# Optimization experiments

Measured on AMD Instinct MI355X. Metric: run time of the kernel, lower is better.

## Reference

```python
import jax, jax.numpy as jnp
import numpy as np

IMAGE_SIZE = 224
IN_CH = 3
A = -0.5
GLIMPSE_SIZES = [12, 23, 68, 135]  # ceil(224 * s) for s in [0.05, 0.1, 0.3, 0.6]
PAD = (GLIMPSE_SIZES[-1] - 1) // 2  # 67
G0 = GLIMPSE_SIZES[0]  # 12 -> all glimpses resized to 12x12
KSIZES = [sz - G0 + 1 for sz in GLIMPSE_SIZES]  # [1, 12, 57, 124]
BATCH = 256


def _bicubic_kernel(sz, a=A, in_ch=IN_CH, out_ch=1):
    # faithful to GlimpseSensor.init (learn_kernels=False)
    x = np.arange(-sz / 2.0 + 0.5, sz / 2.0 + 0.5)[:, None] * 2.0 / sz * (2.0 if sz > 2.0 else 1.0)
    x = np.abs(x)
    w = np.where(
        x > 2.0,
        0.0,
        np.where(
            x > 1.0,
            a * x**3 - 5.0 * a * x**2 + 8.0 * a * x - 4.0 * a,
            (a + 2.0) * x**3 - (a + 3.0) * x**2 + 1.0,
        ),
    )
    k = w @ w.T  # (sz, sz)
    k = k * out_ch / (in_ch * k.sum())
    return np.broadcast_to(k, (out_ch, in_ch, sz, sz)).astype(np.float32)


def setup_inputs() -> dict:
    key = jax.random.key(0)
    ki, kl = jax.random.split(key)
    imgs = jax.random.normal(ki, (BATCH, IN_CH, IMAGE_SIZE, IMAGE_SIZE), dtype=jnp.float32)
    locs = jax.random.randint(kl, (BATCH, 2), 0, IMAGE_SIZE)
    d = {"imgs": imgs, "locs": locs}
    for i, sz in enumerate(KSIZES):
        d[f"k{i}"] = jnp.asarray(_bicubic_kernel(sz))
    return d


def _crop(padded_img, loc, g):
    # padded_img: (C, H+2p, W+2p); loc = (x, y); crop rows [p+x-g//2, p+x+(g+1)//2)
    start = (0, PAD + loc[0] - g // 2, PAD + loc[1] - g // 2)
    return jax.lax.dynamic_slice(padded_img, start, (padded_img.shape[0], g, g))


def reference(imgs, locs, k0, k1, k2, k3):
    p = PAD
    padded = jnp.pad(imgs, ((0, 0), (0, 0), (p, p), (p, p)))  # zero padding, as in forward
    kernels = [k0, k1, k2, k3]
    outs = []
    for g, k in zip(GLIMPSE_SIZES, kernels):
        crops = jax.vmap(lambda img, loc: _crop(img, loc, g))(padded, locs)  # (B, C, g, g)
        out = jax.lax.conv_general_dilated(
            crops, k, window_strides=(1, 1), padding='VALID',
            dimension_numbers=('NCHW', 'OIHW', 'NCHW'),
        )  # (B, 1, 12, 12)
        outs.append(out)
    return jnp.concatenate(outs, axis=1)  # (B, num_glimpses, 12, 12)
```

## Files before the change

### kernel.cpp

```cpp
#include <hip/hip_runtime.h>

namespace {

constexpr int IMGSZ = 224;
constexpr int IMG2  = IMGSZ * IMGSZ;

template <int G>
__device__ void chunk_glimpse(
    int b, int gi, int ch,
    const float* __restrict__ img, const int* __restrict__ locs,
    const float* __restrict__ kptr, float* __restrict__ out,
    float (*s_lds)[136], float* vpad, float* upad,
    float (*part2)[16][13], float (*h_lds)[12]) {
  constexpr int KSZ = G - 11;
  constexpr int C0  = KSZ / 2;
  constexpr int G4  = (G + 3) & ~3;
  constexpr int NCB = G4 / 4;
  const int tid = threadIdx.x;
  const int r0 = ch * 16;

  {
    const float rpiv = 1.0f / kptr[C0 * KSZ + C0];
    for (int i = tid; i < 160; i += 128) {
      float v = 0.f;
      const int k = i - 11;
      if (k >= 0 && k < KSZ) v = kptr[C0 * KSZ + k] * rpiv;
      vpad[i] = v;
    }
  }
  for (int i = tid; i < 160; i += 128) {
    float u = 0.f;
    const int j = i - 16;
    if (j >= 0 && j < KSZ) u = kptr[j * KSZ + C0];
    upad[i] = u;
  }

  const int x = locs[2 * b];
  const int y = locs[2 * b + 1];
  const int row0 = x - G / 2 + r0;
  const int col0 = y - G / 2;
  const int R = (G - r0) < 16 ? (G - r0) : 16;
  const float* imgb = img + (size_t)b * (3 * IMG2);

  for (int idx = tid; idx < 16 * G4; idx += 128) {
    const int r = idx / G4;
    const int c = idx - r * G4;
    float s = 0.f;
    if (r < R && c < G) {
      const int row = row0 + r;
      const int col = col0 + c;
      if ((unsigned)row < (unsigned)IMGSZ && (unsigned)col < (unsigned)IMGSZ) {
        const float* p = imgb + row * IMGSZ + col;
        s = p[0] + p[IMG2] + p[2 * IMG2];
      }
    }
    s_lds[r][c] = s;
  }
  __syncthreads();

  const int row = tid & 15;
  const int seg = tid >> 4;
  float acc[12];
  #pragma unroll
  for (int i = 0; i < 12; ++i) acc[i] = 0.f;

  for (int cb = seg; cb < NCB; cb += 8) {
    const int c = cb * 4;
    const float4 s4 = *reinterpret_cast<const float4*>(&s_lds[row][c]);
    float vv[16];
    #pragma unroll
    for (int q = 0; q < 4; ++q) {
      const float4 v4 = *reinterpret_cast<const float4*>(&vpad[c + q * 4]);
      vv[q * 4 + 0] = v4.x; vv[q * 4 + 1] = v4.y; vv[q * 4 + 2] = v4.z; vv[q * 4 + 3] = v4.w;
    }
    const float sj[4] = {s4.x, s4.y, s4.z, s4.w};
    #pragma unroll
    for (int j = 0; j < 4; ++j) {
      #pragma unroll
      for (int ox = 0; ox < 12; ++ox) {
        acc[ox] += sj[j] * vv[11 + j - ox];
      }
    }
  }

  #pragma unroll
  for (int ox = 0; ox < 12; ++ox) {
    acc[ox] += __shfl_down(acc[ox], 32, 64);
    acc[ox] += __shfl_down(acc[ox], 16, 64);
  }
  const int lane = tid & 63;
  const int wv = tid >> 6;
  if (lane < 16) {
    #pragma unroll
    for (int ox = 0; ox < 12; ++ox) part2[wv][lane][ox] = acc[ox];
  }
  __syncthreads();
  for (int e = tid; e < 192; e += 128) {
    const int r = e / 12;
    const int ox = e - r * 12;
    h_lds[r][ox] = (r < R) ? (part2[0][r][ox] + part2[1][r][ox]) : 0.f;
  }
  __syncthreads();

  float* outp = out + ((size_t)b * 4 + gi) * 144;
  #pragma unroll
  for (int pass = 0; pass < 2; ++pass) {
    const int e = tid + pass * 128;
    if (e < 144) {
      const int oy = e / 12;
      const int ox = e - oy * 12;
      float s = 0.f;
      #pragma unroll
      for (int r = 0; r < 16; ++r) {
        s += upad[16 + r0 + r - oy] * h_lds[r][ox];
      }
      atomicAdd(&outp[e], s);
    }
  }
}

__global__ __launch_bounds__(128) void glimpse_kernel(
    const float* __restrict__ img, const int* __restrict__ locs,
    const float* __restrict__ k0, const float* __restrict__ k1,
    const float* __restrict__ k2, const float* __restrict__ k3,
    float* __restrict__ out) {
  __shared__ __align__(16) float s_lds[16][136];
  __shared__ __align__(16) float vpad[160];
  __shared__ __align__(16) float upad[160];
  __shared__ float part2[2][16][13];
  __shared__ float h_lds[16][12];
  const int bid = blockIdx.x;
  const int b = bid & 255;
  const int t = bid >> 8;
  if (t == 0) {
    chunk_glimpse<12 >(b, 0, 0,     img, locs, k0, out, s_lds, vpad, upad, part2, h_lds);
  } else if (t < 3) {
    chunk_glimpse<23 >(b, 1, t - 1, img, locs, k1, out, s_lds, vpad, upad, part2, h_lds);
  } else if (t < 8) {
    chunk_glimpse<68 >(b, 2, t - 3, img, locs, k2, out, s_lds, vpad, upad, part2, h_lds);
  } else {
    chunk_glimpse<135>(b, 3, t - 8, img, locs, k3, out, s_lds, vpad, upad, part2, h_lds);
  }
}

}

extern "C" void kernel_launch(void* const* d_in, const int* in_sizes, int n_in,
                              void* d_out, int out_size, void* d_ws, size_t ws_size,
                              hipStream_t stream) {
  const float* img  = (const float*)d_in[0];
  const int*   locs = (const int*)d_in[1];
  const float* k0   = (const float*)d_in[2];
  const float* k1   = (const float*)d_in[3];
  const float* k2   = (const float*)d_in[4];
  const float* k3   = (const float*)d_in[5];
  float* out = (float*)d_out;

  hipMemsetAsync(out, 0, (size_t)out_size * sizeof(float), stream);
  glimpse_kernel<<<256 * 17, 128, 0, stream>>>(img, locs, k0, k1, k2, k3, out);
}
```

Before: 28.05 us.

## Load image rows directly from global with aligned float4 and make waves independent

The block-wide LDS staging of the channel-summed crop is replaced by per-thread aligned float4 loads straight from global memory. The horizontal kernel vector is pre-shifted by the column misalignment so the loads can be 16-byte aligned, with a scalar path at image edges. Each wave now keeps its own copies of the kernel vectors and the row buffer and issues its own atomicAdds, which removes every __syncthreads in exchange for twice as many atomics per output. A minimum-occupancy hint is also added to the launch bounds.

```diff
diff --git a/kernel.cpp b/kernel.cpp
--- a/kernel.cpp
+++ b/kernel.cpp
@@ -10,75 +10,80 @@
     int b, int gi, int ch,
     const float* __restrict__ img, const int* __restrict__ locs,
     const float* __restrict__ kptr, float* __restrict__ out,
-    float (*s_lds)[136], float* vpad, float* upad,
-    float (*part2)[16][13], float (*h_lds)[12]) {
-  constexpr int KSZ = G - 11;
-  constexpr int C0  = KSZ / 2;
-  constexpr int G4  = (G + 3) & ~3;
-  constexpr int NCB = G4 / 4;
-  const int tid = threadIdx.x;
+    float* __restrict__ vpad2, float* __restrict__ upad,
+    float (*__restrict__ h_lds)[12]) {
+  constexpr int KSZ  = G - 11;
+  constexpr int C0   = KSZ / 2;
+  constexpr int NCB2 = (G + 2) / 4 + 1;
+  const int lane = threadIdx.x & 63;
   const int r0 = ch * 16;
-
-  {
-    const float rpiv = 1.0f / kptr[C0 * KSZ + C0];
-    for (int i = tid; i < 160; i += 128) {
-      float v = 0.f;
-      const int k = i - 11;
-      if (k >= 0 && k < KSZ) v = kptr[C0 * KSZ + k] * rpiv;
-      vpad[i] = v;
-    }
-  }
-  for (int i = tid; i < 160; i += 128) {
-    float u = 0.f;
-    const int j = i - 16;
-    if (j >= 0 && j < KSZ) u = kptr[j * KSZ + C0];
-    upad[i] = u;
-  }
 
   const int x = locs[2 * b];
   const int y = locs[2 * b + 1];
   const int row0 = x - G / 2 + r0;
   const int col0 = y - G / 2;
+  const int sh = col0 & 3;
+  const int col_a0 = col0 - sh;
   const int R = (G - r0) < 16 ? (G - r0) : 16;
   const float* imgb = img + (size_t)b * (3 * IMG2);
 
-  for (int idx = tid; idx < 16 * G4; idx += 128) {
-    const int r = idx / G4;
-    const int c = idx - r * G4;
-    float s = 0.f;
-    if (r < R && c < G) {
-      const int row = row0 + r;
-      const int col = col0 + c;
-      if ((unsigned)row < (unsigned)IMGSZ && (unsigned)col < (unsigned)IMGSZ) {
-        const float* p = imgb + row * IMGSZ + col;
-        s = p[0] + p[IMG2] + p[2 * IMG2];
-      }
+  {
+    const float rpiv = 1.0f / kptr[C0 * KSZ + C0];
+    for (int i = lane; i < 176; i += 64) {
+      const int k = i - 11 - sh;
+      vpad2[i] = (k >= 0 && k < KSZ) ? kptr[C0 * KSZ + k] * rpiv : 0.f;
     }
-    s_lds[r][c] = s;
   }
-  __syncthreads();
+  for (int i = lane; i < 160; i += 64) {
+    const int j = i - 16;
+    upad[i] = (j >= 0 && j < KSZ) ? kptr[j * KSZ + C0] : 0.f;
+  }
 
-  const int row = tid & 15;
-  const int seg = tid >> 4;
+  const int row = lane & 15;
+  const int seg = (threadIdx.x >> 6) * 4 + (lane >> 4);
+
   float acc[12];
   #pragma unroll
   for (int i = 0; i < 12; ++i) acc[i] = 0.f;
 
-  for (int cb = seg; cb < NCB; cb += 8) {
-    const int c = cb * 4;
-    const float4 s4 = *reinterpret_cast<const float4*>(&s_lds[row][c]);
-    float vv[16];
-    #pragma unroll
-    for (int q = 0; q < 4; ++q) {
-      const float4 v4 = *reinterpret_cast<const float4*>(&vpad[c + q * 4]);
-      vv[q * 4 + 0] = v4.x; vv[q * 4 + 1] = v4.y; vv[q * 4 + 2] = v4.z; vv[q * 4 + 3] = v4.w;
-    }
-    const float sj[4] = {s4.x, s4.y, s4.z, s4.w};
-    #pragma unroll
-    for (int j = 0; j < 4; ++j) {
+  const int grow = row0 + row;
+  if (row < R && (unsigned)grow < (unsigned)IMGSZ) {
+    const float* prow = imgb + grow * IMGSZ;
+    const int cend = col0 + G;
+    for (int cb = seg; cb < NCB2; cb += 8) {
+      const int cbase = col_a0 + 4 * cb;
+      if (cbase >= cend) break;
+      float sj[4];
+      if (cbase >= 0 && cbase <= IMGSZ - 4) {
+        const float4 a  = *reinterpret_cast<const float4*>(prow + cbase);
+        const float4 b4 = *reinterpret_cast<const float4*>(prow + IMG2 + cbase);
+        const float4 c4 = *reinterpret_cast<const float4*>(prow + 2 * IMG2 + cbase);
+        sj[0] = a.x + b4.x + c4.x;
+        sj[1] = a.y + b4.y + c4.y;
+        sj[2] = a.z + b4.z + c4.z;
+        sj[3] = a.w + b4.w + c4.w;
+      } else {
+        #pragma unroll
+        for (int j = 0; j < 4; ++j) {
+          const int cc = cbase + j;
+          sj[j] = ((unsigned)cc < (unsigned)IMGSZ)
+                      ? prow[cc] + prow[IMG2 + cc] + prow[2 * IMG2 + cc]
+                      : 0.f;
+        }
+      }
+      float vv[16];
       #pragma unroll
-      for (int ox = 0; ox < 12; ++ox) {
-        acc[ox] += sj[j] * vv[11 + j - ox];
+      for (int q = 0; q < 4; ++q) {
+        const float4 v4 = *reinterpret_cast<const float4*>(vpad2 + 4 * cb + 4 * q);
+        vv[q * 4 + 0] = v4.x; vv[q * 4 + 1] = v4.y;
+        vv[q * 4 + 2] = v4.z; vv[q * 4 + 3] = v4.w;
+      }
+      #pragma unroll
+      for (int j = 0; j < 4; ++j) {
+        #pragma unroll
+        for (int ox = 0; ox < 12; ++ox) {
+          acc[ox] += sj[j] * vv[11 + j - ox];
+        }
       }
     }
   }
@@ -88,58 +93,44 @@
     acc[ox] += __shfl_down(acc[ox], 32, 64);
     acc[ox] += __shfl_down(acc[ox], 16, 64);
   }
-  const int lane = tid & 63;
-  const int wv = tid >> 6;
   if (lane < 16) {
     #pragma unroll
-    for (int ox = 0; ox < 12; ++ox) part2[wv][lane][ox] = acc[ox];
+    for (int ox = 0; ox < 12; ++ox) h_lds[lane][ox] = acc[ox];
   }
-  __syncthreads();
-  for (int e = tid; e < 192; e += 128) {
-    const int r = e / 12;
-    const int ox = e - r * 12;
-    h_lds[r][ox] = (r < R) ? (part2[0][r][ox] + part2[1][r][ox]) : 0.f;
-  }
-  __syncthreads();
 
   float* outp = out + ((size_t)b * 4 + gi) * 144;
-  #pragma unroll
-  for (int pass = 0; pass < 2; ++pass) {
-    const int e = tid + pass * 128;
-    if (e < 144) {
-      const int oy = e / 12;
-      const int ox = e - oy * 12;
-      float s = 0.f;
-      #pragma unroll
-      for (int r = 0; r < 16; ++r) {
-        s += upad[16 + r0 + r - oy] * h_lds[r][ox];
-      }
-      atomicAdd(&outp[e], s);
+  for (int e = lane; e < 144; e += 64) {
+    const int oy = e / 12;
+    const int ox = e - oy * 12;
+    float s = 0.f;
+    #pragma unroll
+    for (int r = 0; r < 16; ++r) {
+      s += upad[16 + r0 + r - oy] * h_lds[r][ox];
     }
+    atomicAdd(&outp[e], s);
   }
 }
 
-__global__ __launch_bounds__(128) void glimpse_kernel(
+__global__ __launch_bounds__(128, 6) void glimpse_kernel(
     const float* __restrict__ img, const int* __restrict__ locs,
     const float* __restrict__ k0, const float* __restrict__ k1,
     const float* __restrict__ k2, const float* __restrict__ k3,
     float* __restrict__ out) {
-  __shared__ __align__(16) float s_lds[16][136];
-  __shared__ __align__(16) float vpad[160];
-  __shared__ __align__(16) float upad[160];
-  __shared__ float part2[2][16][13];
-  __shared__ float h_lds[16][12];
+  __shared__ __align__(16) float vpad2[2][176];
+  __shared__ __align__(16) float upad[2][160];
+  __shared__ float h_lds[2][16][12];
   const int bid = blockIdx.x;
   const int b = bid & 255;
   const int t = bid >> 8;
+  const int wv = threadIdx.x >> 6;
   if (t == 0) {
-    chunk_glimpse<12 >(b, 0, 0,     img, locs, k0, out, s_lds, vpad, upad, part2, h_lds);
+    chunk_glimpse<12 >(b, 0, 0,     img, locs, k0, out, vpad2[wv], upad[wv], h_lds[wv]);
   } else if (t < 3) {
-    chunk_glimpse<23 >(b, 1, t - 1, img, locs, k1, out, s_lds, vpad, upad, part2, h_lds);
+    chunk_glimpse<23 >(b, 1, t - 1, img, locs, k1, out, vpad2[wv], upad[wv], h_lds[wv]);
   } else if (t < 8) {
-    chunk_glimpse<68 >(b, 2, t - 3, img, locs, k2, out, s_lds, vpad, upad, part2, h_lds);
+    chunk_glimpse<68 >(b, 2, t - 3, img, locs, k2, out, vpad2[wv], upad[wv], h_lds[wv]);
   } else {
-    chunk_glimpse<135>(b, 3, t - 8, img, locs, k3, out, s_lds, vpad, upad, part2, h_lds);
+    chunk_glimpse<135>(b, 3, t - 8, img, locs, k3, out, vpad2[wv], upad[wv], h_lds[wv]);
   }
 }
 
```

Result: faster. 27.17 us (median of 2 runs) (-3.1%).
